# Optimization experiments

Measured on AMD Instinct MI355X. Metric: run time of the kernel, lower is better.

## Reference

```python
import jax, jax.numpy as jnp
import numpy as np

HIDDEN = 2048
N_HEADS = 16
N_KV_HEADS = 4
HEAD_DIM = HIDDEN // N_HEADS  # 128
N_GROUPS = N_HEADS // N_KV_HEADS  # 4
ROPE_THETA = 10000.0
B, S = 2, 2048


def setup_inputs() -> dict:
    key = jax.random.key(0)
    k1, k2, k3, k4, k5, k6 = jax.random.split(key, 6)
    hidden_states = jax.random.normal(k1, (B, S, HIDDEN), dtype=jnp.float32)
    position_ids = jnp.sort(jax.random.randint(k2, (B, S), 0, S), axis=-1).astype(jnp.int32)
    scale = 0.02
    Wq = jax.random.normal(k3, (HIDDEN, N_HEADS * HEAD_DIM), dtype=jnp.float32) * scale
    Wk = jax.random.normal(k4, (HIDDEN, N_KV_HEADS * HEAD_DIM), dtype=jnp.float32) * scale
    Wv = jax.random.normal(k5, (HIDDEN, N_KV_HEADS * HEAD_DIM), dtype=jnp.float32) * scale
    Wo = jax.random.normal(k6, (HIDDEN, HIDDEN), dtype=jnp.float32) * scale
    return {"hidden_states": hidden_states, "position_ids": position_ids,
            "Wq": Wq, "Wk": Wk, "Wv": Wv, "Wo": Wo}


def _rotate_half(x):
    x1, x2 = jnp.split(x, 2, axis=-1)
    return jnp.concatenate([-x2, x1], axis=-1)


def _rope_cos_sin(position_ids, dtype):
    # inv_freq: [HEAD_DIM/2]
    inv_freq = 1.0 / (ROPE_THETA ** (jnp.arange(0, HEAD_DIM, 2, dtype=jnp.float32) / HEAD_DIM))
    # freqs per position: [B, S, HEAD_DIM/2] -> duplicated to [B, S, HEAD_DIM]
    freqs = position_ids.astype(jnp.float32)[..., None] * inv_freq  # [B,S,Dh/2]
    emb = jnp.concatenate([freqs, freqs], axis=-1)  # [B,S,Dh]
    cos = jnp.cos(emb)[:, None, :, :].astype(dtype)  # [B,1,S,Dh]
    sin = jnp.sin(emb)[:, None, :, :].astype(dtype)
    return cos, sin


def reference(hidden_states, position_ids, Wq, Wk, Wv, Wo):
    b, s, _ = hidden_states.shape
    dtype = hidden_states.dtype
    q = (hidden_states @ Wq).reshape(b, s, N_HEADS, HEAD_DIM).transpose(0, 2, 1, 3)      # [B,Hq,S,Dh]
    k = (hidden_states @ Wk).reshape(b, s, N_KV_HEADS, HEAD_DIM).transpose(0, 2, 1, 3)   # [B,Hkv,S,Dh]
    v = (hidden_states @ Wv).reshape(b, s, N_KV_HEADS, HEAD_DIM).transpose(0, 2, 1, 3)

    cos, sin = _rope_cos_sin(position_ids, dtype)
    q = q * cos + _rotate_half(q) * sin
    k = k * cos + _rotate_half(k) * sin

    # repeat_kv: [B,Hkv,S,Dh] -> [B,Hq,S,Dh] (repeat-interleave along head axis)
    k = jnp.repeat(k, N_GROUPS, axis=1)
    v = jnp.repeat(v, N_GROUPS, axis=1)

    scores = jnp.einsum('bhqd,bhkd->bhqk', q, k) / jnp.sqrt(jnp.asarray(HEAD_DIM, dtype))
    # causal additive mask
    causal = jnp.tril(jnp.ones((s, s), dtype=bool))
    scores = jnp.where(causal[None, None], scores, jnp.asarray(-1e9, dtype))
    probs = jax.nn.softmax(scores, axis=-1)
    attn = jnp.einsum('bhqk,bhkd->bhqd', probs, v)  # [B,Hq,S,Dh]
    attn = attn.transpose(0, 2, 1, 3).reshape(b, s, HIDDEN)
    return attn @ Wo
```

## Files before the change

kernel.cpp:

```cpp
#include <hip/hip_runtime.h>
#include <math.h>

#define HID 2048
#define NH 16
#define NKV 4
#define DH 128
#define BB 2
#define SS 2048
#define ROWS (BB*SS)
#define NQKV 3072
#define KOFF 2048
#define VOFF 2560

typedef float f32x4 __attribute__((ext_vector_type(4)));
typedef float f32x16 __attribute__((ext_vector_type(16)));
typedef __bf16 bf16x8 __attribute__((ext_vector_type(8)));
typedef unsigned short ushortx8 __attribute__((ext_vector_type(8)));
typedef unsigned short ushortx4 __attribute__((ext_vector_type(4)));
typedef float floatx4 __attribute__((ext_vector_type(4)));

__device__ __forceinline__ float b2f(unsigned short u) {
  union { float f; unsigned int i; } x; x.i = ((unsigned int)u) << 16; return x.f;
}
__device__ __forceinline__ unsigned short f2b(float f) {
  union { float f; unsigned int i; } x; x.f = f;
  unsigned int r = x.i + 0x7fffu + ((x.i >> 16) & 1u);
  return (unsigned short)(r >> 16);
}

__device__ __forceinline__ void gload16(const void* g, void* l) {
  __builtin_amdgcn_global_load_lds(
      (__attribute__((address_space(1))) void*)(void*)(g),
      (__attribute__((address_space(3))) void*)(l), 16, 0, 0);
}

__device__ __forceinline__ void wgbar() {
  asm volatile("" ::: "memory");
  __builtin_amdgcn_s_barrier();
  asm volatile("" ::: "memory");
}
#define VMCNT4 asm volatile("s_waitcnt vmcnt(4)" ::: "memory")
#define VMCNT3 asm volatile("s_waitcnt vmcnt(3)" ::: "memory")
#define VMCNT0 asm volatile("s_waitcnt vmcnt(0)" ::: "memory")

__device__ __forceinline__ unsigned cvtpk(float lo, float hi_) {
  unsigned r;
  asm("v_cvt_pk_bf16_f32 %0, %1, %2" : "=v"(r) : "v"(lo), "v"(hi_));
  return r;
}
__device__ __forceinline__ void plswap(unsigned& x, unsigned& y) {
  asm volatile("v_permlane32_swap_b32 %0, %1" : "+v"(x), "+v"(y));
}

__global__ __launch_bounds__(256) void cast_f32_bf16(const float* __restrict__ in,
                                                     unsigned short* __restrict__ out, int n4) {
  int i = blockIdx.x * 256 + threadIdx.x;
  if (i >= n4) return;
  floatx4 v = ((const floatx4*)in)[i];
  ushortx4 o;
  o.x = f2b(v.x); o.y = f2b(v.y); o.z = f2b(v.z); o.w = f2b(v.w);
  ((ushortx4*)out)[i] = o;
}

__global__ __launch_bounds__(256) void tcast3(const float* __restrict__ Wq,
                                              const float* __restrict__ Wk,
                                              const float* __restrict__ Wv,
                                              unsigned short* __restrict__ Wt) {
  __shared__ float t[64][65];
  int tid = threadIdx.x;
  int bx = blockIdx.x;
  const float* W; int N, n0; unsigned short* dst;
  if (bx < 32)      { W = Wq; N = 2048; n0 = bx * 64;        dst = Wt; }
  else if (bx < 40) { W = Wk; N = 512;  n0 = (bx - 32) * 64; dst = Wt + (size_t)2048 * 2048; }
  else              { W = Wv; N = 512;  n0 = (bx - 40) * 64; dst = Wt + (size_t)2560 * 2048; }
  int k0 = blockIdx.y * 64;
  const int K = HID;
#pragma unroll
  for (int u0 = 0; u0 < 1024; u0 += 256) {
    int u = u0 + tid;
    int r = u >> 4, c4 = (u & 15) * 4;
    floatx4 v = *(const floatx4*)(const void*)&W[(size_t)(k0 + r) * N + n0 + c4];
    t[r][c4 + 0] = v.x; t[r][c4 + 1] = v.y; t[r][c4 + 2] = v.z; t[r][c4 + 3] = v.w;
  }
  __syncthreads();
#pragma unroll
  for (int u0 = 0; u0 < 512; u0 += 256) {
    int u = u0 + tid;
    int n = u >> 3, g = (u & 7) * 8;
    ushortx8 o;
#pragma unroll
    for (int k2 = 0; k2 < 8; ++k2) o[k2] = f2b(t[g + k2][n]);
    *(ushortx8*)(void*)&dst[(size_t)(n0 + n) * K + k0 + g] = o;
  }
}

__global__ __launch_bounds__(256) void tcast(const float* __restrict__ W,
                                             unsigned short* __restrict__ Wt, int K, int N) {
  __shared__ float t[64][65];
  int tid = threadIdx.x;
  int k0 = blockIdx.y * 64, n0 = blockIdx.x * 64;
#pragma unroll
  for (int u0 = 0; u0 < 1024; u0 += 256) {
    int u = u0 + tid;
    int r = u >> 4, c4 = (u & 15) * 4;
    floatx4 v = *(const floatx4*)(const void*)&W[(size_t)(k0 + r) * N + n0 + c4];
    t[r][c4 + 0] = v.x; t[r][c4 + 1] = v.y; t[r][c4 + 2] = v.z; t[r][c4 + 3] = v.w;
  }
  __syncthreads();
#pragma unroll
  for (int u0 = 0; u0 < 512; u0 += 256) {
    int u = u0 + tid;
    int n = u >> 3, g = (u & 7) * 8;
    ushortx8 o;
#pragma unroll
    for (int k2 = 0; k2 < 8; ++k2) o[k2] = f2b(t[g + k2][n]);
    *(ushortx8*)(void*)&Wt[(size_t)(n0 + n) * K + k0 + g] = o;
  }
}

template <int BF16OUT>
__global__ __launch_bounds__(512, 1) void gemm192n(const unsigned short* __restrict__ A,
                                                   const unsigned short* __restrict__ Bt,
                                                   void* __restrict__ Cv, int M, int N, int K) {
  __shared__ __align__(16) unsigned char smem[131072];
  const int tid = threadIdx.x;
  const int wave = tid >> 6, lane = tid & 63;
  const int fr = lane & 15, fq = lane >> 4;
  const int wm = wave & 3, wn = wave >> 2;

  const int ntn = N / 192;
  const int cpx = gridDim.x >> 3;
  const int wg = (blockIdx.x & 7) * cpx + (blockIdx.x >> 3);
  const int m0 = (wg / ntn) << 8, n0 = (wg % ntn) * 192;
  const int NT = K >> 6;

  const int l8 = lane >> 3, l7 = lane & 7;
  const size_t srcOff = (size_t)(wave * 8 + l8) * K + ((l7 ^ l8) * 8);
  const unsigned short* Ag = A + (size_t)m0 * K;
  const unsigned short* Bg = Bt + (size_t)n0 * K;

  const int cx0 = (fq * 16) ^ ((fr & 7) << 4);
  const int cx1 = (64 + fq * 16) ^ ((fr & 7) << 4);
  const int aRow = (wm * 64 + fr) * 128;
  const int bRow = (wn * 96 + fr) * 128;

#define SA(kt2)  { const unsigned short* gp = Ag + (size_t)(kt2) * 64 + srcOff;              \
    char* lp = (char*)smem + (((kt2) & 1) * 65536) + wave * 1024;                            \
    gload16(gp, lp);                 gload16(gp + (size_t)64 * K, lp + 8192);                \
    gload16(gp + (size_t)128 * K, lp + 16384); gload16(gp + (size_t)192 * K, lp + 24576); }
#define SB(kt2)  { const unsigned short* gp = Bg + (size_t)(kt2) * 64 + srcOff;              \
    char* lp = (char*)smem + (((kt2) & 1) * 65536) + 32768 + wave * 1024;                    \
    gload16(gp, lp);  gload16(gp + (size_t)64 * K, lp + 8192);                               \
    gload16(gp + (size_t)128 * K, lp + 16384); }

  f32x4 acc[4][6] = {};
  bf16x8 aF0[4], aF1[4], bF[6][2];

#define LDA(kf, AF) { const char* b_ = (const char*)smem + cur * 65536 + aRow;               \
    _Pragma("unroll") for (int mi = 0; mi < 4; ++mi)                                         \
      AF[mi] = *(const bf16x8*)(const void*)(b_ + mi * 2048 + ((kf) ? cx1 : cx0)); }
#define LDBALL { const char* b_ = (const char*)smem + cur * 65536 + 32768 + bRow;            \
    _Pragma("unroll") for (int ni = 0; ni < 6; ++ni) {                                       \
      bF[ni][0] = *(const bf16x8*)(const void*)(b_ + ni * 2048 + cx0);                       \
      bF[ni][1] = *(const bf16x8*)(const void*)(b_ + ni * 2048 + cx1); } }
#define MM24(AF, kf) { __builtin_amdgcn_s_setprio(1);                                        \
    _Pragma("unroll") for (int mi = 0; mi < 4; ++mi)                                         \
    _Pragma("unroll") for (int ni = 0; ni < 6; ++ni)                                         \
      acc[mi][ni] = __builtin_amdgcn_mfma_f32_16x16x32_bf16(                                 \
          AF[mi], bF[ni][kf], acc[mi][ni], 0, 0, 0);                                         \
    __builtin_amdgcn_s_setprio(0); }

  SA(0); SB(0); SB(1);
  VMCNT3;
  wgbar();

  for (int kt = 0; kt < NT; ++kt) {
    const int cur = kt & 1;
    LDA(0, aF0); LDBALL;
    if (kt + 1 < NT) SA(kt + 1);
    wgbar();
    MM24(aF0, 0);
    wgbar();
    LDA(1, aF1);
    if (kt + 2 < NT) { SB(kt + 2); VMCNT3; }
    else if (kt + 1 < NT) { VMCNT0; }
    wgbar();
    MM24(aF1, 1);
    wgbar();
  }

#pragma unroll
  for (int mi = 0; mi < 4; ++mi)
#pragma unroll
    for (int ni = 0; ni < 6; ++ni)
#pragma unroll
      for (int r = 0; r < 4; ++r) {
        size_t row = (size_t)(m0 + wm * 64 + mi * 16 + fq * 4 + r);
        size_t col = (size_t)(n0 + wn * 96 + ni * 16 + fr);
        if (BF16OUT)
          ((unsigned short*)Cv)[row * N + col] = f2b(acc[mi][ni][r]);
        else
          ((float*)Cv)[row * N + col] = acc[mi][ni][r];
      }
#undef SA
#undef SB
#undef LDA
#undef LDBALL
#undef MM24
}

template <int BF16OUT>
__global__ __launch_bounds__(512, 1) void gemm128n(const unsigned short* __restrict__ A,
                                                   const unsigned short* __restrict__ Bt,
                                                   void* __restrict__ Cv, int M, int N, int K) {
  __shared__ __align__(16) unsigned char smem[98304];
  const int tid = threadIdx.x;
  const int wave = tid >> 6, lane = tid & 63;
  const int fr = lane & 15, fq = lane >> 4;
  const int wm = wave & 3, wn = wave >> 2;

  const int ntn = N >> 8;
  const int cpx = gridDim.x >> 3;
  const int wg = (blockIdx.x & 7) * cpx + (blockIdx.x >> 3);
  const int m0 = (wg / ntn) << 7, n0 = (wg % ntn) << 8;
  const int NT = K >> 6;

  const int l8 = lane >> 3, l7 = lane & 7;
  const size_t srcOff = (size_t)(wave * 8 + l8) * K + ((l7 ^ l8) * 8);
  const unsigned short* Ag = A + (size_t)m0 * K;
  const unsigned short* Bg = Bt + (size_t)n0 * K;

  const int cx0 = (fq * 16) ^ ((fr & 7) << 4);
  const int cx1 = (64 + fq * 16) ^ ((fr & 7) << 4);
  const int aRow = (wm * 32 + fr) * 128;
  const int bRow = (wn * 128 + fr) * 128;

#define SA(kt2)  { const unsigned short* gp = Ag + (size_t)(kt2) * 64 + srcOff;             \
    char* lp = (char*)smem + (((kt2) & 1) * 49152) + wave * 1024;                           \
    gload16(gp, lp);  gload16(gp + (size_t)64 * K, lp + 8192); }
#define SB01(kt2) { const unsigned short* gp = Bg + (size_t)(kt2) * 64 + srcOff;            \
    char* lp = (char*)smem + (((kt2) & 1) * 49152) + 16384 + wave * 1024;                   \
    gload16(gp, lp);  gload16(gp + (size_t)64 * K, lp + 8192); }
#define SB23(kt2) { const unsigned short* gp = Bg + (size_t)128 * K + (size_t)(kt2) * 64 + srcOff; \
    char* lp = (char*)smem + (((kt2) & 1) * 49152) + 32768 + wave * 1024;                   \
    gload16(gp, lp);  gload16(gp + (size_t)64 * K, lp + 8192); }

  f32x4 acc[2][8] = {};
  bf16x8 aFk[2], bF0[4][2], bF1[4][2];

#define LDAK(kf) { const char* b_ = (const char*)smem + cur * 49152 + aRow;                 \
    aFk[0] = *(const bf16x8*)(const void*)(b_ + ((kf) ? cx1 : cx0));                        \
    aFk[1] = *(const bf16x8*)(const void*)(b_ + 2048 + ((kf) ? cx1 : cx0)); }
#define LDB4(BF, nb) { const char* b_ = (const char*)smem + cur * 49152 + 16384 + bRow + (nb) * 8192; \
    _Pragma("unroll") for (int ni = 0; ni < 4; ++ni) {                                      \
      BF[ni][0] = *(const bf16x8*)(const void*)(b_ + ni * 2048 + cx0);                      \
      BF[ni][1] = *(const bf16x8*)(const void*)(b_ + ni * 2048 + cx1); } }
#define MM8(BF, no, kf) { __builtin_amdgcn_s_setprio(1);                                    \
    _Pragma("unroll") for (int mi = 0; mi < 2; ++mi)                                        \
    _Pragma("unroll") for (int ni = 0; ni < 4; ++ni)                                        \
      acc[mi][(no) + ni] = __builtin_amdgcn_mfma_f32_16x16x32_bf16(                         \
          aFk[mi], BF[ni][kf], acc[mi][(no) + ni], 0, 0, 0);                                \
    __builtin_amdgcn_s_setprio(0); }

  SA(0); SB01(0); SB23(0); SB01(1); SB23(1);
  VMCNT4;
  wgbar();

  for (int kt = 0; kt < NT; ++kt) {
    const int cur = kt & 1;
    LDAK(0); LDB4(bF0, 0); LDB4(bF1, 1);
    if (kt + 1 < NT) SA(kt + 1);
    wgbar();
    MM8(bF0, 0, 0); MM8(bF1, 4, 0);
    wgbar();
    LDAK(1);
    if (kt + 2 < NT) { SB01(kt + 2); SB23(kt + 2); VMCNT4; }
    else if (kt + 1 < NT) { VMCNT0; }
    wgbar();
    MM8(bF0, 0, 1); MM8(bF1, 4, 1);
    wgbar();
  }

#pragma unroll
  for (int mi = 0; mi < 2; ++mi)
#pragma unroll
    for (int ni = 0; ni < 8; ++ni)
#pragma unroll
      for (int r = 0; r < 4; ++r) {
        size_t row = (size_t)(m0 + wm * 32 + mi * 16 + fq * 4 + r);
        size_t col = (size_t)(n0 + wn * 128 + ni * 16 + fr);
        if (BF16OUT)
          ((unsigned short*)Cv)[row * N + col] = f2b(acc[mi][ni][r]);
        else
          ((float*)Cv)[row * N + col] = acc[mi][ni][r];
      }
#undef SA
#undef SB01
#undef SB23
#undef LDAK
#undef LDB4
#undef MM8
}

__global__ __launch_bounds__(256) void rope_kernel(unsigned short* __restrict__ QKV,
                                                   const int* __restrict__ pos) {
  int bs = blockIdx.x;
  int t = threadIdx.x;
  __shared__ float cs[64], sn[64];
  if (t < 64) {
    float p = (float)pos[bs];
    float inv = expf(-(float)t * 0.14391156831212787f);
    sincosf(p * inv, &sn[t], &cs[t]);
  }
  __syncthreads();
  unsigned short* row = QKV + (size_t)bs * NQKV;
  if (t < 160) {
    int h = t >> 3, d0 = (t & 7) * 8;
    int col = (h < 16) ? h * DH : KOFF + (h - 16) * DH;
    float sc = (h < 16) ? 0.08838834764831845f : 1.0f;
    ushortx8 lo = *(const ushortx8*)(const void*)(row + col + d0);
    ushortx8 hi = *(const ushortx8*)(const void*)(row + col + 64 + d0);
    ushortx8 olo, ohi;
#pragma unroll
    for (int k = 0; k < 8; ++k) {
      float x1 = b2f(lo[k]), x2 = b2f(hi[k]);
      float c = cs[d0 + k], s = sn[d0 + k];
      olo[k] = f2b((x1 * c - x2 * s) * sc);
      ohi[k] = f2b((x2 * c + x1 * s) * sc);
    }
    *(ushortx8*)(void*)(row + col + d0) = olo;
    *(ushortx8*)(void*)(row + col + 64 + d0) = ohi;
  }
}

__global__ __launch_bounds__(256) void vtrans(const unsigned short* __restrict__ QKV,
                                              unsigned short* __restrict__ Vt) {
  __shared__ unsigned short t[32][34];
  int s0 = blockIdx.x * 32, d0 = blockIdx.y * 32;
  int bh = blockIdx.z; int b = bh >> 2, h = bh & 3;
  int tx = threadIdx.x & 31, ty = threadIdx.x >> 5;
  const unsigned short* src = QKV + (size_t)b * SS * NQKV + VOFF + h * DH;
  for (int i = 0; i < 32; i += 8)
    t[ty + i][tx] = src[(size_t)(s0 + ty + i) * NQKV + d0 + tx];
  __syncthreads();
  unsigned short* dst = Vt + ((size_t)(b * NKV + h) * DH) * SS;
  for (int i = 0; i < 32; i += 8)
    dst[(size_t)(d0 + ty + i) * SS + s0 + tx] = t[tx][ty + i];
}

__global__ __launch_bounds__(256, 2) void attn_kernel(const unsigned short* __restrict__ QKV,
                                                      const unsigned short* __restrict__ Vt,
                                                      unsigned short* __restrict__ Out) {
  int id = blockIdx.x;
  int g = id & 7;
  int b = g >> 2, hkv = g & 3;
  int r3 = id >> 3;
  int hsub = (r3 >> 2) & 3;
  int h = hkv * 4 + hsub;
  int q0 = (r3 & 3) | (((r3 >> 4) & 1) << 2);
  int qt = (r3 >> 5) ? (15 - q0) : q0;
  int tid = threadIdx.x;
  int w = tid >> 6, lane = tid & 63;
  int l31 = lane & 31, hi = lane >> 5;

  __shared__ __align__(16) unsigned short K_lds[2][64 * 128];
  __shared__ __align__(16) unsigned short V_lds[2][128 * 64];
  __shared__ float lsum_lds[4][32];

  const unsigned short* Kbase = QKV + (size_t)b * SS * NQKV + KOFF + hkv * DH;
  const unsigned short* Vbase = Vt + (size_t)(b * NKV + hkv) * DH * SS;

  int kr4 = lane >> 4, kc = lane & 15;
  int vr8 = lane >> 3, vc = lane & 7;

#define STAGE(kv0, buf)                                                                  \
  { _Pragma("unroll") for (int i = 0; i < 4; ++i) {                                      \
      int r0 = w * 16 + i * 4; int row = r0 + kr4;                                       \
      gload16(Kbase + (size_t)((kv0) + row) * NQKV + ((kc ^ (row & 7)) * 8),             \
              (char*)K_lds[buf] + r0 * 256); }                                           \
    _Pragma("unroll") for (int i = 0; i < 4; ++i) {                                      \
      int r0 = w * 32 + i * 8; int row = r0 + vr8;                                       \
      gload16(Vbase + (size_t)row * SS + (kv0) + ((vc ^ (row & 7)) * 8),                 \
              (char*)V_lds[buf] + r0 * 128); } }

  const unsigned short* Qp =
      QKV + (size_t)((size_t)b * SS + qt * 128 + w * 32 + l31) * NQKV + h * DH + hi * 8;
  bf16x8 qf[8];
#pragma unroll
  for (int ks = 0; ks < 8; ++ks) qf[ks] = *(const bf16x8*)(const void*)(Qp + ks * 16);

  f32x16 o[4] = {};
  float lsum = 0.f;
  int lsw = (l31 & 7) << 4;
  int nt = 2 * qt + 2;

  STAGE(0, 0);
  VMCNT0;
  wgbar();
  int cur = 0;

  for (int t = 0; t < nt; ++t) {
    if (t + 1 < nt) STAGE((t + 1) * 64, cur ^ 1);

    f32x16 s0 = {}, s1 = {};
    {
      const char* kb = (const char*)K_lds[cur];
      __builtin_amdgcn_s_setprio(1);
#pragma unroll
      for (int ks = 0; ks < 8; ++ks) {
        int co = (ks * 32 + hi * 16) ^ lsw;
        bf16x8 k0 = *(const bf16x8*)(const void*)(kb + l31 * 256 + co);
        bf16x8 k1 = *(const bf16x8*)(const void*)(kb + (32 + l31) * 256 + co);
        s0 = __builtin_amdgcn_mfma_f32_32x32x16_bf16(k0, qf[ks], s0, 0, 0, 0);
        s1 = __builtin_amdgcn_mfma_f32_32x32x16_bf16(k1, qf[ks], s1, 0, 0, 0);
      }
      __builtin_amdgcn_s_setprio(0);
    }

    float p0[16], p1[16];
    float ps = 0.f;
    if (t >= 2 * qt) {
      int qrel = w * 32 + l31 - (t - 2 * qt) * 64;
#pragma unroll
      for (int r = 0; r < 16; ++r) {
        int kvr = (r & 3) + 8 * (r >> 2) + 4 * hi;
        float e0 = __expf(s0[r]), e1 = __expf(s1[r]);
        p0[r] = (kvr <= qrel) ? e0 : 0.f;
        p1[r] = (kvr + 32 <= qrel) ? e1 : 0.f;
        ps += p0[r] + p1[r];
      }
    } else {
#pragma unroll
      for (int r = 0; r < 16; ++r) {
        p0[r] = __expf(s0[r]); p1[r] = __expf(s1[r]);
        ps += p0[r] + p1[r];
      }
    }
    lsum += ps;

    union U8 { unsigned u[4]; bf16x8 v; } fa[4];
    {
      unsigned a0 = cvtpk(p0[0], p0[1]),  a1 = cvtpk(p0[2], p0[3]);
      unsigned a2 = cvtpk(p0[4], p0[5]),  a3 = cvtpk(p0[6], p0[7]);
      plswap(a0, a2); plswap(a1, a3);
      fa[0].u[0] = a0; fa[0].u[1] = a1; fa[0].u[2] = a2; fa[0].u[3] = a3;
      unsigned a4 = cvtpk(p0[8], p0[9]),   a5 = cvtpk(p0[10], p0[11]);
      unsigned a6 = cvtpk(p0[12], p0[13]), a7 = cvtpk(p0[14], p0[15]);
      plswap(a4, a6); plswap(a5, a7);
      fa[1].u[0] = a4; fa[1].u[1] = a5; fa[1].u[2] = a6; fa[1].u[3] = a7;
      unsigned b0 = cvtpk(p1[0], p1[1]),  b1 = cvtpk(p1[2], p1[3]);
      unsigned b2 = cvtpk(p1[4], p1[5]),  b3 = cvtpk(p1[6], p1[7]);
      plswap(b0, b2); plswap(b1, b3);
      fa[2].u[0] = b0; fa[2].u[1] = b1; fa[2].u[2] = b2; fa[2].u[3] = b3;
      unsigned b4 = cvtpk(p1[8], p1[9]),   b5 = cvtpk(p1[10], p1[11]);
      unsigned b6 = cvtpk(p1[12], p1[13]), b7 = cvtpk(p1[14], p1[15]);
      plswap(b4, b6); plswap(b5, b7);
      fa[3].u[0] = b4; fa[3].u[1] = b5; fa[3].u[2] = b6; fa[3].u[3] = b7;
    }

    __builtin_amdgcn_s_setprio(1);
#pragma unroll
    for (int dblk = 0; dblk < 4; ++dblk) {
      const char* vrow = (const char*)V_lds[cur] + (dblk * 32 + l31) * 128;
#pragma unroll
      for (int ks = 0; ks < 4; ++ks) {
        bf16x8 vb = *(const bf16x8*)(const void*)(vrow + ((ks * 32 + hi * 16) ^ lsw));
        o[dblk] = __builtin_amdgcn_mfma_f32_32x32x16_bf16(fa[ks].v, vb, o[dblk], 0, 0, 0);
      }
    }
    __builtin_amdgcn_s_setprio(0);

    VMCNT0;
    wgbar();
    cur ^= 1;
  }
#undef STAGE

  float ls = lsum + __shfl_xor(lsum, 32);
  if (hi == 0) lsum_lds[w][l31] = ls;
  __syncthreads();
  size_t obase = (size_t)((size_t)b * SS + qt * 128 + w * 32) * HID + h * DH + l31;
#pragma unroll
  for (int r = 0; r < 16; ++r) {
    int qr = (r & 3) + 8 * (r >> 2) + 4 * hi;
    float inv = 1.0f / lsum_lds[w][qr];
    size_t orow = obase + (size_t)qr * HID;
#pragma unroll
    for (int dblk = 0; dblk < 4; ++dblk)
      Out[orow + dblk * 32] = f2b(o[dblk][r] * inv);
  }
}

extern "C" void kernel_launch(void* const* d_in, const int* in_sizes, int n_in,
                              void* d_out, int out_size, void* d_ws, size_t ws_size,
                              hipStream_t stream) {
  const float* hs = (const float*)d_in[0];
  const int* pos = (const int*)d_in[1];
  const float* Wq = (const float*)d_in[2];
  const float* Wk = (const float*)d_in[3];
  const float* Wv = (const float*)d_in[4];
  const float* Wo = (const float*)d_in[5];

  char* ws = (char*)d_ws;
  size_t off = 0;
  unsigned short* hsb = (unsigned short*)(ws + off); off += (size_t)ROWS * HID * 2;
  unsigned short* WqkvT = (unsigned short*)(ws + off); off += (size_t)NQKV * HID * 2;
  unsigned short* WoT = (unsigned short*)(ws + off); off += (size_t)HID * HID * 2;
  unsigned short* QKV = (unsigned short*)(ws + off); off += (size_t)ROWS * NQKV * 2;
  unsigned short* Vtb = (unsigned short*)(ws + off); off += (size_t)BB * NKV * DH * SS * 2;

  cast_f32_bf16<<<(ROWS * HID / 4 + 255) / 256, 256, 0, stream>>>(hs, hsb, ROWS * HID / 4);
  tcast3<<<dim3(48, HID / 64), 256, 0, stream>>>(Wq, Wk, Wv, WqkvT);
  tcast<<<dim3(HID / 64, HID / 64), 256, 0, stream>>>(Wo, WoT, HID, HID);

  gemm192n<1><<<(ROWS / 256) * (NQKV / 192), 512, 0, stream>>>(hsb, WqkvT, QKV, ROWS, NQKV, HID);
  rope_kernel<<<ROWS, 256, 0, stream>>>(QKV, pos);
  vtrans<<<dim3(SS / 32, DH / 32, BB * NKV), 256, 0, stream>>>(QKV, Vtb);
  attn_kernel<<<512, 256, 0, stream>>>(QKV, Vtb, hsb);
  gemm128n<0><<<(ROWS / 128) * (HID / 256), 512, 0, stream>>>(hsb, WoT, d_out, ROWS, HID, HID);
}
```

Baseline: 185.1 us.

## Split attention KV tile across two wave groups with LDS reduction

The attention block grows from 4 to 8 waves. Each pair of waves shares a 32-row query slice, and each wave of the pair handles one 32-key half of every 64-key tile. This halves the per-wave MFMA and softmax work and the register state per iteration, which should raise the number of waves available to hide latency. The two partial output accumulators and row sums are merged through LDS at the end. That adds a 64KB reduction write and read, and the larger block and LDS footprint may limit how many blocks fit per CU.

```diff
diff --git a/kernel.cpp b/kernel.cpp
--- a/kernel.cpp
+++ b/kernel.cpp
@@ -348,7 +348,7 @@
     dst[(size_t)(d0 + ty + i) * SS + s0 + tx] = t[tx][ty + i];
 }
 
-__global__ __launch_bounds__(256, 2) void attn_kernel(const unsigned short* __restrict__ QKV,
+__global__ __launch_bounds__(512, 4) void attn_kernel(const unsigned short* __restrict__ QKV,
                                                       const unsigned short* __restrict__ Vt,
                                                       unsigned short* __restrict__ Out) {
   int id = blockIdx.x;
@@ -362,10 +362,10 @@
   int tid = threadIdx.x;
   int w = tid >> 6, lane = tid & 63;
   int l31 = lane & 31, hi = lane >> 5;
-
-  __shared__ __align__(16) unsigned short K_lds[2][64 * 128];
-  __shared__ __align__(16) unsigned short V_lds[2][128 * 64];
-  __shared__ float lsum_lds[4][32];
+  int qw = w & 3, kh = w >> 2;
+
+  __shared__ __align__(16) char smem[66560];
+  float* lsumA = (float*)(void*)(smem + 65536);
 
   const unsigned short* Kbase = QKV + (size_t)b * SS * NQKV + KOFF + hkv * DH;
   const unsigned short* Vbase = Vt + (size_t)(b * NKV + hkv) * DH * SS;
@@ -374,17 +374,17 @@
   int vr8 = lane >> 3, vc = lane & 7;
 
 #define STAGE(kv0, buf)                                                                  \
-  { _Pragma("unroll") for (int i = 0; i < 4; ++i) {                                      \
-      int r0 = w * 16 + i * 4; int row = r0 + kr4;                                       \
+  { _Pragma("unroll") for (int i = 0; i < 2; ++i) {                                      \
+      int r0 = w * 8 + i * 4; int row = r0 + kr4;                                        \
       gload16(Kbase + (size_t)((kv0) + row) * NQKV + ((kc ^ (row & 7)) * 8),             \
-              (char*)K_lds[buf] + r0 * 256); }                                           \
-    _Pragma("unroll") for (int i = 0; i < 4; ++i) {                                      \
-      int r0 = w * 32 + i * 8; int row = r0 + vr8;                                       \
+              smem + (buf) * 16384 + r0 * 256); }                                        \
+    _Pragma("unroll") for (int i = 0; i < 2; ++i) {                                      \
+      int r0 = w * 16 + i * 8; int row = r0 + vr8;                                       \
       gload16(Vbase + (size_t)row * SS + (kv0) + ((vc ^ (row & 7)) * 8),                 \
-              (char*)V_lds[buf] + r0 * 128); } }
+              smem + 32768 + (buf) * 16384 + r0 * 128); } }
 
   const unsigned short* Qp =
-      QKV + (size_t)((size_t)b * SS + qt * 128 + w * 32 + l31) * NQKV + h * DH + hi * 8;
+      QKV + (size_t)((size_t)b * SS + qt * 128 + qw * 32 + l31) * NQKV + h * DH + hi * 8;
   bf16x8 qf[8];
 #pragma unroll
   for (int ks = 0; ks < 8; ++ks) qf[ks] = *(const bf16x8*)(const void*)(Qp + ks * 16);
@@ -402,43 +402,36 @@
   for (int t = 0; t < nt; ++t) {
     if (t + 1 < nt) STAGE((t + 1) * 64, cur ^ 1);
 
-    f32x16 s0 = {}, s1 = {};
+    f32x16 s0 = {};
     {
-      const char* kb = (const char*)K_lds[cur];
+      const char* kb = smem + cur * 16384 + (kh * 32 + l31) * 256;
       __builtin_amdgcn_s_setprio(1);
 #pragma unroll
       for (int ks = 0; ks < 8; ++ks) {
-        int co = (ks * 32 + hi * 16) ^ lsw;
-        bf16x8 k0 = *(const bf16x8*)(const void*)(kb + l31 * 256 + co);
-        bf16x8 k1 = *(const bf16x8*)(const void*)(kb + (32 + l31) * 256 + co);
+        bf16x8 k0 = *(const bf16x8*)(const void*)(kb + ((ks * 32 + hi * 16) ^ lsw));
         s0 = __builtin_amdgcn_mfma_f32_32x32x16_bf16(k0, qf[ks], s0, 0, 0, 0);
-        s1 = __builtin_amdgcn_mfma_f32_32x32x16_bf16(k1, qf[ks], s1, 0, 0, 0);
       }
       __builtin_amdgcn_s_setprio(0);
     }
 
-    float p0[16], p1[16];
+    float p0[16];
     float ps = 0.f;
     if (t >= 2 * qt) {
-      int qrel = w * 32 + l31 - (t - 2 * qt) * 64;
+      int qrel = qw * 32 + l31 - (t - 2 * qt) * 64;
 #pragma unroll
       for (int r = 0; r < 16; ++r) {
-        int kvr = (r & 3) + 8 * (r >> 2) + 4 * hi;
-        float e0 = __expf(s0[r]), e1 = __expf(s1[r]);
+        int kvr = (r & 3) + 8 * (r >> 2) + 4 * hi + 32 * kh;
+        float e0 = __expf(s0[r]);
         p0[r] = (kvr <= qrel) ? e0 : 0.f;
-        p1[r] = (kvr + 32 <= qrel) ? e1 : 0.f;
-        ps += p0[r] + p1[r];
+        ps += p0[r];
       }
     } else {
 #pragma unroll
-      for (int r = 0; r < 16; ++r) {
-        p0[r] = __expf(s0[r]); p1[r] = __expf(s1[r]);
-        ps += p0[r] + p1[r];
-      }
+      for (int r = 0; r < 16; ++r) { p0[r] = __expf(s0[r]); ps += p0[r]; }
     }
     lsum += ps;
 
-    union U8 { unsigned u[4]; bf16x8 v; } fa[4];
+    union U8 { unsigned u[4]; bf16x8 v; } fa[2];
     {
       unsigned a0 = cvtpk(p0[0], p0[1]),  a1 = cvtpk(p0[2], p0[3]);
       unsigned a2 = cvtpk(p0[4], p0[5]),  a3 = cvtpk(p0[6], p0[7]);
@@ -448,23 +441,15 @@
       unsigned a6 = cvtpk(p0[12], p0[13]), a7 = cvtpk(p0[14], p0[15]);
       plswap(a4, a6); plswap(a5, a7);
       fa[1].u[0] = a4; fa[1].u[1] = a5; fa[1].u[2] = a6; fa[1].u[3] = a7;
-      unsigned b0 = cvtpk(p1[0], p1[1]),  b1 = cvtpk(p1[2], p1[3]);
-      unsigned b2 = cvtpk(p1[4], p1[5]),  b3 = cvtpk(p1[6], p1[7]);
-      plswap(b0, b2); plswap(b1, b3);
-      fa[2].u[0] = b0; fa[2].u[1] = b1; fa[2].u[2] = b2; fa[2].u[3] = b3;
-      unsigned b4 = cvtpk(p1[8], p1[9]),   b5 = cvtpk(p1[10], p1[11]);
-      unsigned b6 = cvtpk(p1[12], p1[13]), b7 = cvtpk(p1[14], p1[15]);
-      plswap(b4, b6); plswap(b5, b7);
-      fa[3].u[0] = b4; fa[3].u[1] = b5; fa[3].u[2] = b6; fa[3].u[3] = b7;
     }
 
     __builtin_amdgcn_s_setprio(1);
 #pragma unroll
     for (int dblk = 0; dblk < 4; ++dblk) {
-      const char* vrow = (const char*)V_lds[cur] + (dblk * 32 + l31) * 128;
-#pragma unroll
-      for (int ks = 0; ks < 4; ++ks) {
-        bf16x8 vb = *(const bf16x8*)(const void*)(vrow + ((ks * 32 + hi * 16) ^ lsw));
+      const char* vrow = smem + 32768 + cur * 16384 + (dblk * 32 + l31) * 128;
+#pragma unroll
+      for (int ks = 0; ks < 2; ++ks) {
+        bf16x8 vb = *(const bf16x8*)(const void*)(vrow + ((kh * 64 + ks * 32 + hi * 16) ^ lsw));
         o[dblk] = __builtin_amdgcn_mfma_f32_32x32x16_bf16(fa[ks].v, vb, o[dblk], 0, 0, 0);
       }
     }
@@ -477,17 +462,31 @@
 #undef STAGE
 
   float ls = lsum + __shfl_xor(lsum, 32);
-  if (hi == 0) lsum_lds[w][l31] = ls;
+  if (hi == 0) lsumA[w * 32 + l31] = ls;
+  if (kh == 1) {
+    float* rp = (float*)(void*)smem + qw * 4096;
+#pragma unroll
+    for (int r = 0; r < 16; ++r) {
+      int qr = (r & 3) + 8 * (r >> 2) + 4 * hi;
+#pragma unroll
+      for (int dblk = 0; dblk < 4; ++dblk)
+        rp[qr * 128 + dblk * 32 + l31] = o[dblk][r];
+    }
+  }
   __syncthreads();
-  size_t obase = (size_t)((size_t)b * SS + qt * 128 + w * 32) * HID + h * DH + l31;
-#pragma unroll
-  for (int r = 0; r < 16; ++r) {
-    int qr = (r & 3) + 8 * (r >> 2) + 4 * hi;
-    float inv = 1.0f / lsum_lds[w][qr];
-    size_t orow = obase + (size_t)qr * HID;
-#pragma unroll
-    for (int dblk = 0; dblk < 4; ++dblk)
-      Out[orow + dblk * 32] = f2b(o[dblk][r] * inv);
+  if (kh == 0) {
+    const float* rp = (const float*)(void*)smem + qw * 4096;
+    size_t obase = (size_t)((size_t)b * SS + qt * 128 + qw * 32) * HID + h * DH + l31;
+#pragma unroll
+    for (int r = 0; r < 16; ++r) {
+      int qr = (r & 3) + 8 * (r >> 2) + 4 * hi;
+      float tot = lsumA[qw * 32 + qr] + lsumA[(qw + 4) * 32 + qr];
+      float inv = 1.0f / tot;
+      size_t orow = obase + (size_t)qr * HID;
+#pragma unroll
+      for (int dblk = 0; dblk < 4; ++dblk)
+        Out[orow + dblk * 32] = f2b((o[dblk][r] + rp[qr * 128 + dblk * 32 + l31]) * inv);
+    }
   }
 }
 
@@ -516,6 +515,6 @@
   gemm192n<1><<<(ROWS / 256) * (NQKV / 192), 512, 0, stream>>>(hsb, WqkvT, QKV, ROWS, NQKV, HID);
   rope_kernel<<<ROWS, 256, 0, stream>>>(QKV, pos);
   vtrans<<<dim3(SS / 32, DH / 32, BB * NKV), 256, 0, stream>>>(QKV, Vtb);
-  attn_kernel<<<512, 256, 0, stream>>>(QKV, Vtb, hsb);
+  attn_kernel<<<512, 512, 0, stream>>>(QKV, Vtb, hsb);
   gemm128n<0><<<(ROWS / 128) * (HID / 256), 512, 0, stream>>>(hsb, WoT, d_out, ROWS, HID, HID);
 }
```

Measured after the change: 240.0 us. +29.6%, slower.
